# Optimization experiments

Hardware: AMD Instinct MI355X
Metric: run time of the kernel (lower is better)

## Reference

```python
import jax, jax.numpy as jnp
import numpy as np

B, LQ, LK = 4, 2048, 2048
XS, YS, PD = 1024, 1024, 128


def setup_inputs() -> dict:
    key = jax.random.key(0)
    ks = jax.random.split(key, 8)
    s_x = 1.0 / np.sqrt(XS)
    s_y = 1.0 / np.sqrt(YS)
    return {
        "x": jax.random.normal(ks[0], (B, LQ, XS), dtype=jnp.float32),
        "y": jax.random.normal(ks[1], (B, LK, YS), dtype=jnp.float32),
        "Wq": jax.random.normal(ks[2], (XS, PD), dtype=jnp.float32) * s_x,
        "bq": jax.random.normal(ks[3], (PD,), dtype=jnp.float32) * 0.01,
        "Wk": jax.random.normal(ks[4], (YS, PD), dtype=jnp.float32) * s_y,
        "bk": jax.random.normal(ks[5], (PD,), dtype=jnp.float32) * 0.01,
        "Wv": jax.random.normal(ks[6], (YS, PD), dtype=jnp.float32) * s_y,
        "bv": jax.random.normal(ks[7], (PD,), dtype=jnp.float32) * 0.01,
        "mask": 1,
    }


def reference(x, y, Wq, bq, Wk, bk, Wv, bv, mask):
    # Projections (torch Linear: x @ W^T + b; here weights stored as [in, out])
    q = x @ Wq + bq  # [B, LQ, PD]
    k = y @ Wk + bk  # [B, LK, PD]
    v = y @ Wv + bv  # [B, LK, PD]
    scale = 1.0 / jnp.sqrt(jnp.asarray(PD, dtype=q.dtype))
    att = jax.nn.softmax(jnp.einsum("bqd,bkd->bqk", q, k) * scale, axis=-1)
    if mask:
        # NOTE: faithful to original — triu applied AFTER softmax (diagonal=1),
        # zeroing the lower triangle + diagonal without renormalizing.
        att = jnp.triu(att, k=1)
    return jnp.einsum("bqk,bkd->bqd", att, v)  # [B, LQ, PD]
```

## Files before the change

### kernel.cpp

```cpp
#include <hip/hip_runtime.h>

typedef short s8v __attribute__((ext_vector_type(8)));
typedef float f4v __attribute__((ext_vector_type(4)));

#define NB 4
#define LQ 2048
#define LKK 2048
#define XS 1024
#define PDD 128

#define PST 68
#define AST 132

__device__ __forceinline__ ushort f2bf(float x) {
  union { float f; uint u; } v; v.f = x;
  uint r = (v.u + 0x7fffu + ((v.u >> 16) & 1u)) >> 16;
  return (ushort)r;
}

__global__ __launch_bounds__(256) void k_wtrans(const float* __restrict__ Wq,
                                                const float* __restrict__ Wk,
                                                const float* __restrict__ Wv,
                                                ushort* __restrict__ Wt) {
  int p = blockIdx.y;
  const float* W = (p == 0) ? Wq : (p == 1) ? Wk : Wv;
  ushort* out = Wt + (size_t)p * (PDD * XS);
  int t = threadIdx.x;
  int n = t >> 1;
  int kk0 = (t & 1) * 16;
  int k0 = blockIdx.x * 32;
  ushort tmp[16];
#pragma unroll
  for (int i = 0; i < 16; ++i) tmp[i] = f2bf(W[(size_t)(k0 + kk0 + i) * PDD + n]);
  uint4 u0, u1;
  u0.x = tmp[0] | ((uint)tmp[1] << 16);  u0.y = tmp[2] | ((uint)tmp[3] << 16);
  u0.z = tmp[4] | ((uint)tmp[5] << 16);  u0.w = tmp[6] | ((uint)tmp[7] << 16);
  u1.x = tmp[8] | ((uint)tmp[9] << 16);  u1.y = tmp[10] | ((uint)tmp[11] << 16);
  u1.z = tmp[12] | ((uint)tmp[13] << 16); u1.w = tmp[14] | ((uint)tmp[15] << 16);
  uint4* dst = (uint4*)&out[n * XS + k0 + kk0];
  dst[0] = u0; dst[1] = u1;
}

__global__ __launch_bounds__(256) void k_proj(const float* __restrict__ x,
                                              const float* __restrict__ y,
                                              const ushort* __restrict__ Wt,
                                              const float* __restrict__ bq,
                                              const float* __restrict__ bk,
                                              const float* __restrict__ bv,
                                              ushort* __restrict__ qo,
                                              ushort* __restrict__ ko,
                                              ushort* __restrict__ vt) {
  int p = blockIdx.y;
  const float* in = (p == 0) ? x : y;
  const ushort* wt = Wt + (size_t)p * (PDD * XS);
  int row0 = blockIdx.x * 64;
  __shared__ ushort As[64 * 72];
  __shared__ ushort Bs[128 * 72];
  int t = threadIdx.x, wave = t >> 6, lane = t & 63, quad = lane >> 4, lc = lane & 15;
  const f4v z4 = {0.f, 0.f, 0.f, 0.f};
  f4v acc[8];
#pragma unroll
  for (int i = 0; i < 8; ++i) acc[i] = z4;
  for (int k0 = 0; k0 < XS; k0 += 64) {
    {
      int r = t >> 2, c0 = (t & 3) * 16;
      const float* src = in + (size_t)(row0 + r) * XS + k0 + c0;
      float4 a0 = *(const float4*)src;
      float4 a1 = *(const float4*)(src + 4);
      float4 a2 = *(const float4*)(src + 8);
      float4 a3 = *(const float4*)(src + 12);
      uint4 p0, p1;
      p0.x = f2bf(a0.x) | ((uint)f2bf(a0.y) << 16);
      p0.y = f2bf(a0.z) | ((uint)f2bf(a0.w) << 16);
      p0.z = f2bf(a1.x) | ((uint)f2bf(a1.y) << 16);
      p0.w = f2bf(a1.z) | ((uint)f2bf(a1.w) << 16);
      p1.x = f2bf(a2.x) | ((uint)f2bf(a2.y) << 16);
      p1.y = f2bf(a2.z) | ((uint)f2bf(a2.w) << 16);
      p1.z = f2bf(a3.x) | ((uint)f2bf(a3.y) << 16);
      p1.w = f2bf(a3.z) | ((uint)f2bf(a3.w) << 16);
      *(uint4*)&As[r * 72 + c0] = p0;
      *(uint4*)&As[r * 72 + c0 + 8] = p1;
    }
    {
      int n = t >> 1, kk0 = (t & 1) * 32;
      const ushort* s0 = wt + (size_t)n * XS + k0 + kk0;
      uint4 u0 = *(const uint4*)s0;
      uint4 u1 = *(const uint4*)(s0 + 8);
      uint4 u2 = *(const uint4*)(s0 + 16);
      uint4 u3 = *(const uint4*)(s0 + 24);
      *(uint4*)&Bs[n * 72 + kk0] = u0;
      *(uint4*)&Bs[n * 72 + kk0 + 8] = u1;
      *(uint4*)&Bs[n * 72 + kk0 + 16] = u2;
      *(uint4*)&Bs[n * 72 + kk0 + 24] = u3;
    }
    __syncthreads();
#pragma unroll
    for (int kc = 0; kc < 2; ++kc) {
      s8v a = *(const s8v*)&As[(wave * 16 + lc) * 72 + kc * 32 + quad * 8];
#pragma unroll
      for (int nt = 0; nt < 8; ++nt) {
        s8v bfr = *(const s8v*)&Bs[(nt * 16 + lc) * 72 + kc * 32 + quad * 8];
        acc[nt] = __builtin_amdgcn_mfma_f32_16x16x32_bf16(a, bfr, acc[nt], 0, 0, 0);
      }
    }
    __syncthreads();
  }
  const float qscale = 0.08838834764831845f;
  const float* bias = (p == 0) ? bq : (p == 1) ? bk : bv;
  if (p < 2) {
    ushort* o = (p == 0) ? qo : ko;
    float scl = (p == 0) ? qscale : 1.0f;
#pragma unroll
    for (int nt = 0; nt < 8; ++nt) {
      int col = nt * 16 + lc;
      float bb = bias[col];
#pragma unroll
      for (int g = 0; g < 4; ++g) {
        int r = row0 + wave * 16 + quad * 4 + g;
        o[(size_t)r * PDD + col] = f2bf((acc[nt][g] + bb) * scl);
      }
    }
  } else {
    int rbase = row0 + wave * 16 + quad * 4;
    int b = rbase >> 11, rr = rbase & 2047;
#pragma unroll
    for (int nt = 0; nt < 8; ++nt) {
      int col = nt * 16 + lc;
      float bb = bias[col];
      ushort4 pk;
      pk.x = f2bf(acc[nt][0] + bb);
      pk.y = f2bf(acc[nt][1] + bb);
      pk.z = f2bf(acc[nt][2] + bb);
      pk.w = f2bf(acc[nt][3] + bb);
      *(ushort4*)&vt[((size_t)(b * PDD + col)) * LKK + rr] = pk;
    }
  }
}

__global__ __launch_bounds__(512, 2) void k_attn(const ushort* __restrict__ qg,
                                                 const ushort* __restrict__ kg,
                                                 const ushort* __restrict__ vtg,
                                                 const int* __restrict__ maskp,
                                                 float* __restrict__ out) {
  __shared__ float smem[8 * 32 * PST];
  __shared__ float lS[8][2][16];
  int bx = blockIdx.x;
  int xcd = bx & 7;
  int b = xcd >> 1;
  int q0 = ((bx >> 3) * 2 + (xcd & 1)) * 32;
  int t = threadIdx.x;
  int wave = t >> 6, lane = t & 63, quad = lane >> 4, lc = lane & 15;
  int domask = *maskp;
  float* Psw = smem + wave * (32 * PST);

  s8v aq[2][4];
#pragma unroll
  for (int m = 0; m < 2; ++m) {
    const ushort* qrow = qg + ((size_t)(b * LQ + q0 + m * 16 + lc)) * PDD + quad * 8;
#pragma unroll
    for (int kc = 0; kc < 4; ++kc) aq[m][kc] = *(const s8v*)(qrow + kc * 32);
  }

  const f4v z4 = {0.f, 0.f, 0.f, 0.f};
  f4v acc[2][8];
#pragma unroll
  for (int m = 0; m < 2; ++m)
#pragma unroll
    for (int i = 0; i < 8; ++i) acc[m][i] = z4;
  float rs[2][4] = {{0.f, 0.f, 0.f, 0.f}, {0.f, 0.f, 0.f, 0.f}};

  const ushort* kbase = kg + ((size_t)(b * LKK + wave * 64 + lc)) * PDD + quad * 8;
  const ushort* vbase = vtg + ((size_t)(b * PDD + lc)) * LKK + wave * 64 + quad * 8;

#pragma unroll 1
  for (int i = 0; i < 4; ++i) {
    int kt = wave + i * 8;
    const ushort* kp = kbase + (size_t)(i * 512) * PDD;
    f4v sf[2][4];
#pragma unroll
    for (int nt = 0; nt < 4; ++nt) {
      s8v kf[4];
#pragma unroll
      for (int kc = 0; kc < 4; ++kc)
        kf[kc] = *(const s8v*)(kp + (size_t)(nt * 16) * PDD + kc * 32);
      f4v s0 = z4, s1 = z4;
#pragma unroll
      for (int kc = 0; kc < 4; ++kc) {
        s0 = __builtin_amdgcn_mfma_f32_16x16x32_bf16(aq[0][kc], kf[kc], s0, 0, 0, 0);
        s1 = __builtin_amdgcn_mfma_f32_16x16x32_bf16(aq[1][kc], kf[kc], s1, 0, 0, 0);
      }
      sf[0][nt] = s0;
      sf[1][nt] = s1;
    }

    s8v vf0[8];
#pragma unroll
    for (int dt = 0; dt < 8; ++dt)
      vf0[dt] = *(const s8v*)(vbase + (size_t)(dt * 16) * LKK + i * 512);

#pragma unroll
    for (int m = 0; m < 2; ++m)
#pragma unroll
      for (int g = 0; g < 4; ++g) {
        int rg = q0 + m * 16 + quad * 4 + g;
#pragma unroll
        for (int nt = 0; nt < 4; ++nt) {
          float pv = __expf(sf[m][nt][g]);
          rs[m][g] += pv;
          int jg = kt * 64 + nt * 16 + lc;
          if (domask && (jg <= rg)) pv = 0.f;
          Psw[(m * 16 + quad * 4 + g) * PST + nt * 16 + lc] = pv;
        }
      }

    s8v vf1[8];
#pragma unroll
    for (int dt = 0; dt < 8; ++dt)
      vf1[dt] = *(const s8v*)(vbase + (size_t)(dt * 16) * LKK + i * 512 + 32);

#pragma unroll
    for (int jc = 0; jc < 2; ++jc)
#pragma unroll
      for (int m = 0; m < 2; ++m) {
        const float* pp = &Psw[(m * 16 + lc) * PST + jc * 32 + quad * 8];
        float4 p0 = *(const float4*)pp;
        float4 p1 = *(const float4*)(pp + 4);
        s8v ap;
        ap[0] = (short)f2bf(p0.x); ap[1] = (short)f2bf(p0.y);
        ap[2] = (short)f2bf(p0.z); ap[3] = (short)f2bf(p0.w);
        ap[4] = (short)f2bf(p1.x); ap[5] = (short)f2bf(p1.y);
        ap[6] = (short)f2bf(p1.z); ap[7] = (short)f2bf(p1.w);
#pragma unroll
        for (int dt = 0; dt < 8; ++dt) {
          s8v bv4 = jc ? vf1[dt] : vf0[dt];
          acc[m][dt] = __builtin_amdgcn_mfma_f32_16x16x32_bf16(ap, bv4, acc[m][dt], 0, 0, 0);
        }
      }
  }

#pragma unroll
  for (int off = 8; off >= 1; off >>= 1)
#pragma unroll
    for (int m = 0; m < 2; ++m)
#pragma unroll
      for (int g = 0; g < 4; ++g) rs[m][g] += __shfl_xor(rs[m][g], off, 64);

  __syncthreads();
  if (lc == 0) {
#pragma unroll
    for (int m = 0; m < 2; ++m)
#pragma unroll
      for (int g = 0; g < 4; ++g) lS[wave][m][quad * 4 + g] = rs[m][g];
  }

#pragma unroll
  for (int m = 0; m < 2; ++m) {
#pragma unroll
    for (int dt = 0; dt < 8; ++dt)
#pragma unroll
      for (int g = 0; g < 4; ++g)
        smem[wave * (16 * AST) + (quad * 4 + g) * AST + dt * 16 + lc] = acc[m][dt][g];
    __syncthreads();
    {
      int row = t >> 5, c0 = (t & 31) * 4;
      float L = 0.f;
      float ox = 0.f, oy = 0.f, oz = 0.f, ow = 0.f;
#pragma unroll
      for (int p = 0; p < 8; ++p) {
        L += lS[p][m][row];
        const float* a = &smem[p * (16 * AST) + row * AST + c0];
        float4 xv = *(const float4*)a;
        ox += xv.x; oy += xv.y; oz += xv.z; ow += xv.w;
      }
      float inv = 1.0f / L;
      float4 o;
      o.x = ox * inv; o.y = oy * inv; o.z = oz * inv; o.w = ow * inv;
      float* op = out + ((size_t)(b * LQ + q0 + m * 16 + row)) * PDD + c0;
      *(float4*)op = o;
    }
    __syncthreads();
  }
}

extern "C" void kernel_launch(void* const* d_in, const int* in_sizes, int n_in,
                              void* d_out, int out_size, void* d_ws, size_t ws_size,
                              hipStream_t stream) {
  const float* x  = (const float*)d_in[0];
  const float* y  = (const float*)d_in[1];
  const float* Wq = (const float*)d_in[2];
  const float* bq = (const float*)d_in[3];
  const float* Wk = (const float*)d_in[4];
  const float* bk = (const float*)d_in[5];
  const float* Wv = (const float*)d_in[6];
  const float* bv = (const float*)d_in[7];
  const int* mask = (const int*)d_in[8];
  char* ws = (char*)d_ws;
  ushort* qb = (ushort*)(ws);
  ushort* kb = (ushort*)(ws + (size_t)(1 << 21));
  ushort* vt = (ushort*)(ws + (size_t)(2 << 21));
  ushort* Wt = (ushort*)(ws + (size_t)(3 << 21));
  float* out = (float*)d_out;

  hipLaunchKernelGGL(k_wtrans, dim3(32, 3), dim3(256), 0, stream, Wq, Wk, Wv, Wt);
  hipLaunchKernelGGL(k_proj, dim3(128, 3), dim3(256), 0, stream, x, y, Wt, bq, bk, bv, qb, kb, vt);
  hipLaunchKernelGGL(k_attn, dim3(256), dim3(512), 0, stream, qb, kb, vt, mask, out);
}
```

Baseline: 169.7 us.

## Rewrite projection GEMM to load fragments directly into registers with double buffering

The projection kernel no longer stages A and B tiles through shared memory with barriers. Each wave now loads its MFMA operand fragments straight from global memory into registers, converts fp32 to bf16 in registers, and uses a two-stage register double buffer so the next K-slab's loads overlap the current MFMAs. Waves are retiled into a 2x2 layout of 32 rows by 64 columns, and the grid is flattened to one dimension. The aim is to remove LDS traffic and syncthreads stalls, at the cost of more register pressure and less coalesced global loads with weight rows re-read per wave.

```diff
diff --git a/kernel.cpp b/kernel.cpp
--- a/kernel.cpp
+++ b/kernel.cpp
@@ -41,98 +41,120 @@
   dst[0] = u0; dst[1] = u1;
 }
 
-__global__ __launch_bounds__(256) void k_proj(const float* __restrict__ x,
-                                              const float* __restrict__ y,
-                                              const ushort* __restrict__ Wt,
-                                              const float* __restrict__ bq,
-                                              const float* __restrict__ bk,
-                                              const float* __restrict__ bv,
-                                              ushort* __restrict__ qo,
-                                              ushort* __restrict__ ko,
-                                              ushort* __restrict__ vt) {
-  int p = blockIdx.y;
+__global__ __launch_bounds__(256, 1) void k_proj(const float* __restrict__ x,
+                                                 const float* __restrict__ y,
+                                                 const ushort* __restrict__ Wt,
+                                                 const float* __restrict__ bq,
+                                                 const float* __restrict__ bk,
+                                                 const float* __restrict__ bv,
+                                                 ushort* __restrict__ qo,
+                                                 ushort* __restrict__ ko,
+                                                 ushort* __restrict__ vt) {
+  int bx = blockIdx.x;
+  int p = bx >> 7;
+  int tile = bx & 127;
   const float* in = (p == 0) ? x : y;
   const ushort* wt = Wt + (size_t)p * (PDD * XS);
-  int row0 = blockIdx.x * 64;
-  __shared__ ushort As[64 * 72];
-  __shared__ ushort Bs[128 * 72];
   int t = threadIdx.x, wave = t >> 6, lane = t & 63, quad = lane >> 4, lc = lane & 15;
+  int row0 = tile * 64 + (wave & 1) * 32;
+  int nc0 = (wave >> 1) * 64;
+
+  const float* arow0 = in + (size_t)(row0 + lc) * XS + quad * 8;
+  const float* arow1 = in + (size_t)(row0 + 16 + lc) * XS + quad * 8;
+  const ushort* brow0 = wt + (size_t)(nc0 + 0 * 16 + lc) * XS + quad * 8;
+  const ushort* brow1 = wt + (size_t)(nc0 + 1 * 16 + lc) * XS + quad * 8;
+  const ushort* brow2 = wt + (size_t)(nc0 + 2 * 16 + lc) * XS + quad * 8;
+  const ushort* brow3 = wt + (size_t)(nc0 + 3 * 16 + lc) * XS + quad * 8;
+
   const f4v z4 = {0.f, 0.f, 0.f, 0.f};
-  f4v acc[8];
-#pragma unroll
-  for (int i = 0; i < 8; ++i) acc[i] = z4;
-  for (int k0 = 0; k0 < XS; k0 += 64) {
-    {
-      int r = t >> 2, c0 = (t & 3) * 16;
-      const float* src = in + (size_t)(row0 + r) * XS + k0 + c0;
-      float4 a0 = *(const float4*)src;
-      float4 a1 = *(const float4*)(src + 4);
-      float4 a2 = *(const float4*)(src + 8);
-      float4 a3 = *(const float4*)(src + 12);
-      uint4 p0, p1;
-      p0.x = f2bf(a0.x) | ((uint)f2bf(a0.y) << 16);
-      p0.y = f2bf(a0.z) | ((uint)f2bf(a0.w) << 16);
-      p0.z = f2bf(a1.x) | ((uint)f2bf(a1.y) << 16);
-      p0.w = f2bf(a1.z) | ((uint)f2bf(a1.w) << 16);
-      p1.x = f2bf(a2.x) | ((uint)f2bf(a2.y) << 16);
-      p1.y = f2bf(a2.z) | ((uint)f2bf(a2.w) << 16);
-      p1.z = f2bf(a3.x) | ((uint)f2bf(a3.y) << 16);
-      p1.w = f2bf(a3.z) | ((uint)f2bf(a3.w) << 16);
-      *(uint4*)&As[r * 72 + c0] = p0;
-      *(uint4*)&As[r * 72 + c0 + 8] = p1;
-    }
-    {
-      int n = t >> 1, kk0 = (t & 1) * 32;
-      const ushort* s0 = wt + (size_t)n * XS + k0 + kk0;
-      uint4 u0 = *(const uint4*)s0;
-      uint4 u1 = *(const uint4*)(s0 + 8);
-      uint4 u2 = *(const uint4*)(s0 + 16);
-      uint4 u3 = *(const uint4*)(s0 + 24);
-      *(uint4*)&Bs[n * 72 + kk0] = u0;
-      *(uint4*)&Bs[n * 72 + kk0 + 8] = u1;
-      *(uint4*)&Bs[n * 72 + kk0 + 16] = u2;
-      *(uint4*)&Bs[n * 72 + kk0 + 24] = u3;
-    }
-    __syncthreads();
-#pragma unroll
-    for (int kc = 0; kc < 2; ++kc) {
-      s8v a = *(const s8v*)&As[(wave * 16 + lc) * 72 + kc * 32 + quad * 8];
-#pragma unroll
-      for (int nt = 0; nt < 8; ++nt) {
-        s8v bfr = *(const s8v*)&Bs[(nt * 16 + lc) * 72 + kc * 32 + quad * 8];
-        acc[nt] = __builtin_amdgcn_mfma_f32_16x16x32_bf16(a, bfr, acc[nt], 0, 0, 0);
-      }
-    }
-    __syncthreads();
-  }
+  f4v acc[2][4];
+#pragma unroll
+  for (int m = 0; m < 2; ++m)
+#pragma unroll
+    for (int n = 0; n < 4; ++n) acc[m][n] = z4;
+
+  auto pack8 = [](const float4& lo, const float4& hi) {
+    s8v r;
+    r[0] = (short)f2bf(lo.x); r[1] = (short)f2bf(lo.y);
+    r[2] = (short)f2bf(lo.z); r[3] = (short)f2bf(lo.w);
+    r[4] = (short)f2bf(hi.x); r[5] = (short)f2bf(hi.y);
+    r[6] = (short)f2bf(hi.z); r[7] = (short)f2bf(hi.w);
+    return r;
+  };
+
+  auto pload = [&](float4 (&Ab)[2][2][2], s8v (&Bb)[4][2], int koff) {
+    const float* a0 = arow0 + koff;
+    const float* a1 = arow1 + koff;
+    Ab[0][0][0] = *(const float4*)a0;        Ab[0][0][1] = *(const float4*)(a0 + 4);
+    Ab[0][1][0] = *(const float4*)(a0 + 32); Ab[0][1][1] = *(const float4*)(a0 + 36);
+    Ab[1][0][0] = *(const float4*)a1;        Ab[1][0][1] = *(const float4*)(a1 + 4);
+    Ab[1][1][0] = *(const float4*)(a1 + 32); Ab[1][1][1] = *(const float4*)(a1 + 36);
+    Bb[0][0] = *(const s8v*)(brow0 + koff);  Bb[0][1] = *(const s8v*)(brow0 + koff + 32);
+    Bb[1][0] = *(const s8v*)(brow1 + koff);  Bb[1][1] = *(const s8v*)(brow1 + koff + 32);
+    Bb[2][0] = *(const s8v*)(brow2 + koff);  Bb[2][1] = *(const s8v*)(brow2 + koff + 32);
+    Bb[3][0] = *(const s8v*)(brow3 + koff);  Bb[3][1] = *(const s8v*)(brow3 + koff + 32);
+  };
+
+  auto pcomp = [&](float4 (&Ab)[2][2][2], s8v (&Bb)[4][2]) {
+    s8v aq[2][2];
+#pragma unroll
+    for (int m = 0; m < 2; ++m)
+#pragma unroll
+      for (int kc = 0; kc < 2; ++kc) aq[m][kc] = pack8(Ab[m][kc][0], Ab[m][kc][1]);
+#pragma unroll
+    for (int kc = 0; kc < 2; ++kc)
+#pragma unroll
+      for (int m = 0; m < 2; ++m)
+#pragma unroll
+        for (int n = 0; n < 4; ++n)
+          acc[m][n] = __builtin_amdgcn_mfma_f32_16x16x32_bf16(aq[m][kc], Bb[n][kc], acc[m][n], 0, 0, 0);
+  };
+
+  float4 A0[2][2][2], A1[2][2][2];
+  s8v B0[4][2], B1[4][2];
+  pload(A0, B0, 0);
+#pragma unroll 1
+  for (int k0 = 0; k0 < XS; k0 += 128) {
+    pload(A1, B1, k0 + 64);
+    pcomp(A0, B0);
+    int kn = (k0 + 128) & (XS - 1);
+    pload(A0, B0, kn);
+    pcomp(A1, B1);
+  }
+
   const float qscale = 0.08838834764831845f;
   const float* bias = (p == 0) ? bq : (p == 1) ? bk : bv;
   if (p < 2) {
     ushort* o = (p == 0) ? qo : ko;
     float scl = (p == 0) ? qscale : 1.0f;
 #pragma unroll
-    for (int nt = 0; nt < 8; ++nt) {
-      int col = nt * 16 + lc;
-      float bb = bias[col];
-#pragma unroll
-      for (int g = 0; g < 4; ++g) {
-        int r = row0 + wave * 16 + quad * 4 + g;
-        o[(size_t)r * PDD + col] = f2bf((acc[nt][g] + bb) * scl);
-      }
-    }
+    for (int m = 0; m < 2; ++m)
+#pragma unroll
+      for (int n = 0; n < 4; ++n) {
+        int col = nc0 + n * 16 + lc;
+        float bb = bias[col];
+#pragma unroll
+        for (int g = 0; g < 4; ++g) {
+          int r = row0 + m * 16 + quad * 4 + g;
+          o[(size_t)r * PDD + col] = f2bf((acc[m][n][g] + bb) * scl);
+        }
+      }
   } else {
-    int rbase = row0 + wave * 16 + quad * 4;
-    int b = rbase >> 11, rr = rbase & 2047;
-#pragma unroll
-    for (int nt = 0; nt < 8; ++nt) {
-      int col = nt * 16 + lc;
-      float bb = bias[col];
-      ushort4 pk;
-      pk.x = f2bf(acc[nt][0] + bb);
-      pk.y = f2bf(acc[nt][1] + bb);
-      pk.z = f2bf(acc[nt][2] + bb);
-      pk.w = f2bf(acc[nt][3] + bb);
-      *(ushort4*)&vt[((size_t)(b * PDD + col)) * LKK + rr] = pk;
+#pragma unroll
+    for (int m = 0; m < 2; ++m) {
+      int rbase = row0 + m * 16 + quad * 4;
+      int b = rbase >> 11, rr = rbase & 2047;
+#pragma unroll
+      for (int n = 0; n < 4; ++n) {
+        int col = nc0 + n * 16 + lc;
+        float bb = bias[col];
+        ushort4 pk;
+        pk.x = f2bf(acc[m][n][0] + bb);
+        pk.y = f2bf(acc[m][n][1] + bb);
+        pk.z = f2bf(acc[m][n][2] + bb);
+        pk.w = f2bf(acc[m][n][3] + bb);
+        *(ushort4*)&vt[((size_t)(b * PDD + col)) * LKK + rr] = pk;
+      }
     }
   }
 }
@@ -302,6 +324,6 @@
   float* out = (float*)d_out;
 
   hipLaunchKernelGGL(k_wtrans, dim3(32, 3), dim3(256), 0, stream, Wq, Wk, Wv, Wt);
-  hipLaunchKernelGGL(k_proj, dim3(128, 3), dim3(256), 0, stream, x, y, Wt, bq, bk, bv, qb, kb, vt);
+  hipLaunchKernelGGL(k_proj, dim3(384), dim3(256), 0, stream, x, y, Wt, bq, bk, bv, qb, kb, vt);
   hipLaunchKernelGGL(k_attn, dim3(256), dim3(512), 0, stream, qb, kb, vt, mask, out);
 }
```

Result: slower. 195.0 us (+14.9%).
